# Performance work log

Measured on AMD Instinct MI355X. Metric: run time of the kernel, lower is better.

Reference implementation:

```python
import jax, jax.numpy as jnp
import numpy as np
from jax import lax

B_, K_, T_, V_ = 2, 4, 1024, 1024
D_MODEL, EXPAND = 512, 2
D_INNER = EXPAND * D_MODEL          # 1024
N_STATE, D_CONV, DT_RANK, L_ = 16, 4, 32, 2


def setup_inputs() -> dict:
    key = jax.random.key(0)
    ks = jax.random.split(key, 9)
    s = 0.02
    A0 = jnp.log(jnp.arange(1, N_STATE + 1, dtype=jnp.float32))  # S4D-real init
    return {
        'codes': jax.random.randint(ks[0], (B_, K_, T_), 0, V_),
        'embed_w': jax.random.normal(ks[1], (K_, V_, D_MODEL), jnp.float32) * s,
        'norm_w': jnp.ones((L_, D_MODEL), jnp.float32),
        'in_proj_w': jax.random.normal(ks[2], (L_, 2 * D_INNER, D_MODEL), jnp.float32) * s,
        'conv_w': jax.random.normal(ks[3], (L_, D_INNER, 1, D_CONV), jnp.float32) * s,
        'conv_b': jnp.zeros((L_, D_INNER), jnp.float32),
        'x_proj_w': jax.random.normal(ks[4], (L_, DT_RANK + 2 * N_STATE, D_INNER), jnp.float32) * s,
        'dt_proj_w': jax.random.normal(ks[5], (L_, D_INNER, DT_RANK), jnp.float32) * s,
        'dt_proj_b': jnp.zeros((L_, D_INNER), jnp.float32),
        'A_log': jnp.broadcast_to(A0, (L_, D_INNER, N_STATE)) + 0.0,
        'D_skip': jnp.ones((L_, D_INNER), jnp.float32),
        'out_proj_w': jax.random.normal(ks[6], (L_, D_MODEL, D_INNER), jnp.float32) * s,
        'head_w': jax.random.normal(ks[7], (K_, D_MODEL, V_), jnp.float32) * s,
    }


def rmsnorm(x, w, eps=1e-6):
    return x * w * lax.rsqrt(jnp.mean(x * x, axis=-1, keepdims=True) + eps)


def causal_dwconv(x, w, b):
    # x: (B,T,D); w: (D,1,d_conv) depthwise; torch pads d_conv-1 both sides then slices [:T]
    # == left-pad-only causal conv.
    xt = x.transpose(0, 2, 1)  # (B,D,T)
    y = lax.conv_general_dilated(xt, w, (1,), [(D_CONV - 1, 0)],
                                 feature_group_count=D_INNER,
                                 dimension_numbers=('NCH', 'OIH', 'NCH'))
    return (y + b[None, :, None]).transpose(0, 2, 1)


def mamba_block(x, norm_w, in_w, cw, cb, xp_w, dtp_w, dtp_b, A_log, D_skip, out_w):
    res = x
    x = rmsnorm(x, norm_w)
    xz = x @ in_w.T                                   # (B,T,2*d_inner)
    x_ssm, z = jnp.split(xz, 2, axis=-1)
    x_ssm = jax.nn.silu(causal_dwconv(x_ssm, cw, cb))  # (B,T,D)
    x_dbl = x_ssm @ xp_w.T                            # (B,T,dt_rank+2N)
    dt_lr, Bm, Cm = jnp.split(x_dbl, [DT_RANK, DT_RANK + N_STATE], axis=-1)
    dt = jax.nn.softplus(dt_lr @ dtp_w.T + dtp_b)     # (B,T,D)
    A = -jnp.exp(A_log)                               # (D,N)
    dA = jnp.exp(dt[..., None] * A)                   # (B,T,D,N)
    dBx = dt[..., None] * Bm[:, :, None, :] * x_ssm[..., None]  # (B,T,D,N)

    def step(h, inp):
        dA_t, dBx_t, C_t = inp
        h = dA_t * h + dBx_t                          # (B,D,N)
        return h, jnp.einsum('bdn,bn->bd', h, C_t)

    h0 = jnp.zeros((x.shape[0], D_INNER, N_STATE), x.dtype)
    _, ys = lax.scan(step, h0, (dA.transpose(1, 0, 2, 3),
                                dBx.transpose(1, 0, 2, 3),
                                Cm.transpose(1, 0, 2)))
    y = ys.transpose(1, 0, 2) + x_ssm * D_skip        # (B,T,D)
    y = y * jax.nn.silu(z)
    return res + y @ out_w.T


def reference(codes, embed_w, norm_w, in_proj_w, conv_w, conv_b, x_proj_w,
              dt_proj_w, dt_proj_b, A_log, D_skip, out_proj_w, head_w):
    k_idx = jnp.arange(K_)[None, :, None]
    x = embed_w[k_idx, codes].sum(axis=1)             # (B,T,d_model): RVQ sum-embedding
    for l in range(L_):
        x = mamba_block(x, norm_w[l], in_proj_w[l], conv_w[l], conv_b[l],
                        x_proj_w[l], dt_proj_w[l], dt_proj_b[l],
                        A_log[l], D_skip[l], out_proj_w[l])
    return jnp.einsum('btd,kdv->bktv', x, head_w)     # (B,K,T,V)
```

## Files before the change

### kernel.cpp

```cpp
#include <hip/hip_runtime.h>
#include <hip/hip_bf16.h>


#define B_SZ 2
#define K_CB 4
#define T_SZ 1024
#define V_SZ 1024
#define DM 512
#define DI 1024
#define NS 16
#define DTR 32
#define NCHUNK 64
#define TCHUNK 16

typedef unsigned short u16;
typedef long long ll;
using short8 = __attribute__((ext_vector_type(8))) short;
using f32x4  = __attribute__((ext_vector_type(4))) float;

__device__ __forceinline__ float bf2f(u16 u) {
    union { unsigned int i; float f; } v; v.i = ((unsigned int)u) << 16; return v.f;
}
__device__ __forceinline__ u16 f2bf(float f) {
    union { float f; unsigned int i; } v; v.f = f;
    unsigned int x = v.i;
    return (u16)((x + 0x7fffu + ((x >> 16) & 1u)) >> 16);
}
__device__ __forceinline__ float siluf(float x) { return x / (1.f + __expf(-x)); }
__device__ __forceinline__ float softplusf(float x) { return (x > 20.f) ? x : log1pf(__expf(x)); }

__global__ __launch_bounds__(256) void mega0_k(const float* __restrict__ in_w,
                                               const float* __restrict__ xp_w,
                                               const float* __restrict__ dtp_w,
                                               const float* __restrict__ out_w,
                                               u16* __restrict__ w_in, u16* __restrict__ w_xp,
                                               u16* __restrict__ w_dt, u16* __restrict__ w_out,
                                               const float* __restrict__ head_w,
                                               u16* __restrict__ w_hd,
                                               const int* __restrict__ codes,
                                               const float* __restrict__ ew,
                                               const float* __restrict__ nw,
                                               float* __restrict__ x,
                                               u16* __restrict__ xn) {
    __shared__ float tile[64][65];
    int bid = blockIdx.x;
    int tid = threadIdx.x;
    if (bid < 3264) {
        int i = (bid * 256 + tid) << 2;
        const float* s; u16* d;
        if (i < 2097152) { s = in_w + i; d = w_in + i; }
        else {
            i -= 2097152;
            if (i < 131072) { s = xp_w + i; d = w_xp + i; }
            else {
                i -= 131072;
                if (i < 65536) { s = dtp_w + i; d = w_dt + i; }
                else { i -= 65536; s = out_w + i; d = w_out + i; }
            }
        }
        float4 v = *(const float4*)s;
        ushort4 o; o.x = f2bf(v.x); o.y = f2bf(v.y); o.z = f2bf(v.z); o.w = f2bf(v.w);
        *(ushort4*)d = o;
    } else if (bid < 3776) {
        int idx = bid - 3264;
        int z = idx >> 7, rest = idx & 127;
        int d0 = (rest >> 4) << 6, v0 = (rest & 15) << 6;
        int col = tid & 63, rbase = tid >> 6;
#pragma unroll
        for (int i = 0; i < 16; i++) {
            int row = (i << 2) + rbase;
            tile[row][col] = head_w[(ll)z * (DM * V_SZ) + (ll)(d0 + row) * V_SZ + v0 + col];
        }
        __syncthreads();
#pragma unroll
        for (int i = 0; i < 16; i++) {
            int vrow = (i << 2) + rbase;
            w_hd[(ll)z * (V_SZ * DM) + (ll)(v0 + vrow) * DM + d0 + col] = f2bf(tile[col][vrow]);
        }
    } else {
        int row = bid - 3776;
        int b = row >> 10, t = row & 1023;
        float a0 = 0.f, a1 = 0.f;
#pragma unroll
        for (int k = 0; k < K_CB; k++) {
            int c = codes[b * (K_CB * T_SZ) + k * T_SZ + t];
            a0 += ew[((ll)k * V_SZ + c) * DM + tid];
            a1 += ew[((ll)k * V_SZ + c) * DM + tid + 256];
        }
        x[(ll)row * DM + tid]       = a0;
        x[(ll)row * DM + tid + 256] = a1;
        float ss = a0 * a0 + a1 * a1;
#pragma unroll
        for (int off = 32; off > 0; off >>= 1) ss += __shfl_down(ss, off, 64);
        float* red = &tile[0][0];
        if ((tid & 63) == 0) red[tid >> 6] = ss;
        __syncthreads();
        float tot = red[0] + red[1] + red[2] + red[3];
        float scale = rsqrtf(tot * (1.0f / DM) + 1e-6f);
        xn[(ll)row * DM + tid]       = f2bf(a0 * scale * nw[tid]);
        xn[(ll)row * DM + tid + 256] = f2bf(a1 * scale * nw[tid + 256]);
    }
}

__global__ __launch_bounds__(256) void rmsnorm_k(const float* __restrict__ x,
                                                 const float* __restrict__ w,
                                                 u16* __restrict__ xn) {
    ll row = blockIdx.x;
    const float* xr = x + row * DM;
    int tid = threadIdx.x;
    float v0 = xr[tid], v1 = xr[tid + 256];
    float ss = v0 * v0 + v1 * v1;
#pragma unroll
    for (int off = 32; off > 0; off >>= 1) ss += __shfl_down(ss, off, 64);
    __shared__ float red[4];
    if ((tid & 63) == 0) red[tid >> 6] = ss;
    __syncthreads();
    float tot = red[0] + red[1] + red[2] + red[3];
    float scale = rsqrtf(tot * (1.0f / DM) + 1e-6f);
    xn[row * DM + tid]       = f2bf(v0 * scale * w[tid]);
    xn[row * DM + tid + 256] = f2bf(v1 * scale * w[tid + 256]);
}

template <int EP>
__global__ __launch_bounds__(256) void mgemm2_k(const u16* __restrict__ A, int lda,
                                                const u16* __restrict__ W,
                                                float* __restrict__ C,
                                                u16* __restrict__ Cb, int ldcb, int K) {
    __shared__ u16 As[2][4096];
    __shared__ u16 Bs[2][4096];
    int tid = threadIdx.x;
    int wave = tid >> 6, lane = tid & 63;
    int q = lane >> 4, r = lane & 15;
    int m0 = blockIdx.y << 7, n0 = blockIdx.x << 7;
    int wm = (wave >> 1) << 6, wn = (wave & 1) << 6;
    int srow = tid >> 1, soff = (tid & 1) << 4;
    const u16* Ap = A + (ll)(m0 + srow) * lda + soff;
    const u16* Wp = W + (ll)(n0 + srow) * K + soff;
    int sidx = (srow << 5) + soff;
    f32x4 acc[4][4];
#pragma unroll
    for (int i = 0; i < 4; i++)
#pragma unroll
        for (int j = 0; j < 4; j++) acc[i][j] = (f32x4){0.f, 0.f, 0.f, 0.f};

    uint4 ra0 = *(const uint4*)Ap,       ra1 = *(const uint4*)(Ap + 8);
    uint4 rb0 = *(const uint4*)Wp,       rb1 = *(const uint4*)(Wp + 8);
    *(uint4*)&As[0][sidx] = ra0; *(uint4*)&As[0][sidx + 8] = ra1;
    *(uint4*)&Bs[0][sidx] = rb0; *(uint4*)&Bs[0][sidx + 8] = rb1;
    __syncthreads();

    int p = 0;
    for (int k0 = 0; k0 < K; k0 += 32) {
        bool pf = (k0 + 32) < K;
        if (pf) {
            ra0 = *(const uint4*)(Ap + k0 + 32); ra1 = *(const uint4*)(Ap + k0 + 40);
            rb0 = *(const uint4*)(Wp + k0 + 32); rb1 = *(const uint4*)(Wp + k0 + 40);
        }
        short8 af[4], bfr[4];
#pragma unroll
        for (int i = 0; i < 4; i++) af[i]  = *(const short8*)&As[p][((wm + (i << 4) + r) << 5) + (q << 3)];
#pragma unroll
        for (int j = 0; j < 4; j++) bfr[j] = *(const short8*)&Bs[p][((wn + (j << 4) + r) << 5) + (q << 3)];
#pragma unroll
        for (int i = 0; i < 4; i++)
#pragma unroll
            for (int j = 0; j < 4; j++)
                acc[i][j] = __builtin_amdgcn_mfma_f32_16x16x32_bf16(af[i], bfr[j], acc[i][j], 0, 0, 0);
        if (pf) {
            *(uint4*)&As[p ^ 1][sidx] = ra0; *(uint4*)&As[p ^ 1][sidx + 8] = ra1;
            *(uint4*)&Bs[p ^ 1][sidx] = rb0; *(uint4*)&Bs[p ^ 1][sidx + 8] = rb1;
        }
        __syncthreads();
        p ^= 1;
    }

#pragma unroll
    for (int i = 0; i < 4; i++)
#pragma unroll
        for (int j = 0; j < 4; j++)
#pragma unroll
            for (int g = 0; g < 4; g++) {
                int m = m0 + wm + (i << 4) + (q << 2) + g;
                int n = n0 + wn + (j << 4) + r;
                float v = acc[i][j][g];
                if (EP == 0) {
                    Cb[(ll)m * ldcb + n] = f2bf(v);
                } else {
                    int z = n >> 10, vv = n & 1023;
                    int b = m >> 10, t = m & 1023;
                    C[((ll)(b * K_CB + z) * T_SZ + t) * V_SZ + vv] = v;
                }
            }
}

template <int EP>
__global__ __launch_bounds__(256) void mgemm_k(const u16* __restrict__ A, int lda,
                                               const u16* __restrict__ W,
                                               float* __restrict__ C, int ldc, int K,
                                               const float* __restrict__ bias,
                                               u16* __restrict__ Cb, int ldcb) {
    __shared__ u16 As[2][2048];
    __shared__ u16 Bs[2][2048];
    int tid = threadIdx.x;
    int m0 = blockIdx.y << 6, n0 = blockIdx.x << 6;
    int lane = tid & 63, wave = tid >> 6;
    int q = lane >> 4, r = lane & 15;
    int wm = (wave >> 1) << 5, wn = (wave & 1) << 5;
    int srow = tid >> 2, soff = (tid & 3) << 3;
    const u16* Ap = A + (ll)(m0 + srow) * lda + soff;
    const u16* Wp = W + (ll)(n0 + srow) * K + soff;
    int sidx = (srow << 5) + soff;
    f32x4 acc[2][2];
#pragma unroll
    for (int i = 0; i < 2; i++)
#pragma unroll
        for (int j = 0; j < 2; j++) acc[i][j] = (f32x4){0.f, 0.f, 0.f, 0.f};

    uint4 ra = *(const uint4*)Ap;
    uint4 rb = *(const uint4*)Wp;
    *(uint4*)&As[0][sidx] = ra;
    *(uint4*)&Bs[0][sidx] = rb;
    __syncthreads();

    int p = 0;
    for (int k0 = 0; k0 < K; k0 += 32) {
        bool pf = (k0 + 32) < K;
        if (pf) {
            ra = *(const uint4*)(Ap + k0 + 32);
            rb = *(const uint4*)(Wp + k0 + 32);
        }
        short8 af[2], bfr[2];
#pragma unroll
        for (int i = 0; i < 2; i++) af[i]  = *(const short8*)&As[p][((wm + (i << 4) + r) << 5) + (q << 3)];
#pragma unroll
        for (int j = 0; j < 2; j++) bfr[j] = *(const short8*)&Bs[p][((wn + (j << 4) + r) << 5) + (q << 3)];
#pragma unroll
        for (int i = 0; i < 2; i++)
#pragma unroll
            for (int j = 0; j < 2; j++)
                acc[i][j] = __builtin_amdgcn_mfma_f32_16x16x32_bf16(af[i], bfr[j], acc[i][j], 0, 0, 0);
        if (pf) {
            *(uint4*)&As[p ^ 1][sidx] = ra;
            *(uint4*)&Bs[p ^ 1][sidx] = rb;
        }
        __syncthreads();
        p ^= 1;
    }

#pragma unroll
    for (int i = 0; i < 2; i++)
#pragma unroll
        for (int j = 0; j < 2; j++)
#pragma unroll
            for (int g = 0; g < 4; g++) {
                int m = m0 + wm + (i << 4) + (q << 2) + g;
                int n = n0 + wn + (j << 4) + r;
                float v = acc[i][j][g];
                float nv = C[(ll)m * ldc + n] + v;
                C[(ll)m * ldc + n] = nv;
                Cb[(ll)m * ldcb + n] = f2bf(nv);
            }
}

__global__ __launch_bounds__(256) void convxp_k(const u16* __restrict__ xzb,
                                                const float* __restrict__ cw,
                                                const float* __restrict__ cb,
                                                const u16* __restrict__ W,
                                                float* __restrict__ xc,
                                                float* __restrict__ xdbl,
                                                u16* __restrict__ xdbl_bf) {
    __shared__ u16 xcs[16][1032];
    __shared__ u16 Bs[2][2048];
    int blk = blockIdx.x, tid = threadIdx.x;
    int b = blk >> 6, tg = blk & 63;
    int t0 = tg << 4;
    ll ro0 = (ll)b * T_SZ + t0;
    int c0 = tid << 2;
    float4 a = *(const float4*)&cb[c0];
    float4 cwv[4];
#pragma unroll
    for (int e = 0; e < 4; e++) cwv[e] = *(const float4*)&cw[(c0 + e) << 2];
    ushort4 v[19];
#pragma unroll
    for (int i = 0; i < 19; i++) {
        int t = t0 - 3 + i;
        if (t >= 0) v[i] = *(const ushort4*)&xzb[((ll)(b * T_SZ + t)) * (2 * DI) + c0];
        else        v[i] = (ushort4){0, 0, 0, 0};
    }
#pragma unroll
    for (int tr = 0; tr < 16; tr++) {
        float acc0 = a.x, acc1 = a.y, acc2 = a.z, acc3 = a.w;
#pragma unroll
        for (int j = 0; j < 4; j++) {
            ushort4 vv = v[tr + j];
            acc0 = fmaf(bf2f(vv.x), ((const float*)&cwv[0])[j], acc0);
            acc1 = fmaf(bf2f(vv.y), ((const float*)&cwv[1])[j], acc1);
            acc2 = fmaf(bf2f(vv.z), ((const float*)&cwv[2])[j], acc2);
            acc3 = fmaf(bf2f(vv.w), ((const float*)&cwv[3])[j], acc3);
        }
        float4 s; ushort4 sb;
        s.x = siluf(acc0); s.y = siluf(acc1); s.z = siluf(acc2); s.w = siluf(acc3);
        sb.x = f2bf(s.x); sb.y = f2bf(s.y); sb.z = f2bf(s.z); sb.w = f2bf(s.w);
        *(float4*)&xc[(ro0 + tr) * DI + c0] = s;
        *(ushort4*)&xcs[tr][c0] = sb;
    }
    __syncthreads();

    int lane = tid & 63, wave = tid >> 6;
    int q = lane >> 4, r = lane & 15;
    int srow = tid >> 2, soff = (tid & 3) << 3;
    f32x4 acc = (f32x4){0.f, 0.f, 0.f, 0.f};
    uint4 rb = *(const uint4*)(W + (ll)srow * DI + soff);
    *(uint4*)&Bs[0][(srow << 5) + soff] = rb;
    __syncthreads();
    int p = 0;
    for (int k0 = 0; k0 < DI; k0 += 32) {
        bool pf = (k0 + 32) < DI;
        if (pf) rb = *(const uint4*)(W + (ll)srow * DI + k0 + 32 + soff);
        short8 af  = *(const short8*)&xcs[r][k0 + (q << 3)];
        short8 bfr = *(const short8*)&Bs[p][(((wave << 4) + r) << 5) + (q << 3)];
        acc = __builtin_amdgcn_mfma_f32_16x16x32_bf16(af, bfr, acc, 0, 0, 0);
        if (pf) *(uint4*)&Bs[p ^ 1][(srow << 5) + soff] = rb;
        __syncthreads();
        p ^= 1;
    }
#pragma unroll
    for (int g = 0; g < 4; g++) {
        int tr = (q << 2) + g;
        int n = (wave << 4) + r;
        float vv = acc[g];
        xdbl[(ro0 + tr) * 64 + n]    = vv;
        xdbl_bf[(ro0 + tr) * 64 + n] = f2bf(vv);
    }
}

__global__ __launch_bounds__(256) void dtscan1_k(const u16* __restrict__ A,
                                                 const u16* __restrict__ W,
                                                 const float* __restrict__ bias,
                                                 const float* __restrict__ xc,
                                                 const float* __restrict__ xdbl,
                                                 const float* __restrict__ A_log,
                                                 float* __restrict__ dtb,
                                                 float* __restrict__ pA,
                                                 float* __restrict__ U) {
    __shared__ u16 As[2048];
    __shared__ u16 Bs[2048];
    __shared__ float dts[64][65];
    __shared__ float BCs[64][16];
    int tid = threadIdx.x;
    int m0 = blockIdx.y << 6, n0 = blockIdx.x << 6;
    int lane = tid & 63, wave = tid >> 6;
    int q = lane >> 4, r = lane & 15;
    int wm = (wave >> 1) << 5, wn = (wave & 1) << 5;
    {
        int srow = tid >> 2, soff = (tid & 3) << 3;
        *(uint4*)&As[(srow << 5) + soff] = *(const uint4*)(A + (ll)(m0 + srow) * 64 + soff);
        *(uint4*)&Bs[(srow << 5) + soff] = *(const uint4*)(W + (ll)(n0 + srow) * DTR + soff);
        int rr = tid >> 2, cc = (tid & 3) << 2;
        *(float4*)&BCs[rr][cc] = *(const float4*)&xdbl[(ll)(m0 + rr) * 64 + DTR + cc];
    }
    int sd = lane;
    int sc = wave;
    int dg = n0 + sd;
    float Av[NS];
#pragma unroll
    for (int n4 = 0; n4 < 4; n4++) {
        float4 alv = *(const float4*)&A_log[dg * NS + (n4 << 2)];
        Av[(n4 << 2) + 0] = -__expf(alv.x); Av[(n4 << 2) + 1] = -__expf(alv.y);
        Av[(n4 << 2) + 2] = -__expf(alv.z); Av[(n4 << 2) + 3] = -__expf(alv.w);
    }
    __syncthreads();

    f32x4 acc[2][2];
#pragma unroll
    for (int i = 0; i < 2; i++)
#pragma unroll
        for (int j = 0; j < 2; j++) acc[i][j] = (f32x4){0.f, 0.f, 0.f, 0.f};
    short8 af[2], bfr[2];
#pragma unroll
    for (int i = 0; i < 2; i++) af[i]  = *(const short8*)&As[((wm + (i << 4) + r) << 5) + (q << 3)];
#pragma unroll
    for (int j = 0; j < 2; j++) bfr[j] = *(const short8*)&Bs[((wn + (j << 4) + r) << 5) + (q << 3)];
#pragma unroll
    for (int i = 0; i < 2; i++)
#pragma unroll
        for (int j = 0; j < 2; j++)
            acc[i][j] = __builtin_amdgcn_mfma_f32_16x16x32_bf16(af[i], bfr[j], acc[i][j], 0, 0, 0);

#pragma unroll
    for (int i = 0; i < 2; i++)
#pragma unroll
        for (int j = 0; j < 2; j++)
#pragma unroll
            for (int g = 0; g < 4; g++) {
                int mm = wm + (i << 4) + (q << 2) + g;
                int nn = wn + (j << 4) + r;
                float dtl = softplusf(acc[i][j][g] + bias[n0 + nn]);
                dtb[(ll)(m0 + mm) * DI + (n0 + nn)] = dtl;
                dts[mm][nn] = dtl;
            }
    __syncthreads();

    int b = m0 >> 10;
    int c = ((m0 & 1023) >> 4) + sc;
    int tl0 = sc << 4;
    float p[NS], u[NS];
#pragma unroll
    for (int n = 0; n < NS; n++) { p[n] = 1.f; u[n] = 0.f; }
#pragma unroll
    for (int s = 0; s < TCHUNK; s++) {
        int tl = tl0 + s;
        float dtv = dts[tl][sd];
        float xv = xc[(ll)(m0 + tl) * DI + dg];
        float dx = dtv * xv;
#pragma unroll
        for (int n = 0; n < NS; n++) {
            float aa = __expf(dtv * Av[n]);
            p[n] *= aa;
            u[n] = fmaf(aa, u[n], dx * BCs[tl][n]);
        }
    }
    ll o = ((ll)b * NCHUNK + c) * (NS * DI) + dg;
#pragma unroll
    for (int n = 0; n < NS; n++) { pA[o + n * DI] = p[n]; U[o + n * DI] = u[n]; }
}

__global__ __launch_bounds__(256) void scan2_k(const float* __restrict__ pA,
                                               const float* __restrict__ U,
                                               float* __restrict__ hst) {
    int i = blockIdx.x * 256 + threadIdx.x;
    int b = i >> 14;
    int rest = i & 16383;
    float h = 0.f;
#pragma unroll
    for (int c = 0; c < NCHUNK; c++) {
        ll o = ((ll)b * NCHUNK + c) * (DI * NS) + rest;
        float pa = pA[o], u = U[o];
        hst[o] = h;
        h = fmaf(pa, h, u);
    }
}

__global__ __launch_bounds__(256) void scan3_k(const float* __restrict__ dt,
                                               const float* __restrict__ xc,
                                               const float* __restrict__ xdbl,
                                               const u16* __restrict__ xzb,
                                               const float* __restrict__ A_log,
                                               const float* __restrict__ Dk,
                                               const float* __restrict__ hst,
                                               u16* __restrict__ y) {
    int blk = blockIdx.x;
    int dblk = blk & 3;
    int c = (blk >> 2) & (NCHUNK - 1);
    int b = blk >> 8;
    int d = dblk * 256 + threadIdx.x;
    int t0 = c * TCHUNK;
    __shared__ float BC[TCHUNK][32];
    if (threadIdx.x < TCHUNK * 8) {
        int rr = threadIdx.x >> 3, cc = (threadIdx.x & 7) << 2;
        *(float4*)&BC[rr][cc] = *(const float4*)&xdbl[((ll)(b * T_SZ + t0 + rr)) * 64 + DTR + cc];
    }
    float Av[NS];
#pragma unroll
    for (int n4 = 0; n4 < 4; n4++) {
        float4 alv = *(const float4*)&A_log[d * NS + (n4 << 2)];
        Av[(n4 << 2) + 0] = -__expf(alv.x); Av[(n4 << 2) + 1] = -__expf(alv.y);
        Av[(n4 << 2) + 2] = -__expf(alv.z); Av[(n4 << 2) + 3] = -__expf(alv.w);
    }
    float h[NS];
    ll ho = (((ll)b * NCHUNK + c) * (NS * DI)) + d;
#pragma unroll
    for (int n = 0; n < NS; n++) h[n] = hst[ho + n * DI];
    float Dv = Dk[d];
    __syncthreads();
#pragma unroll
    for (int s = 0; s < TCHUNK; s++) {
        ll ro = (ll)(b * T_SZ + t0 + s);
        float dtv = dt[ro * DI + d];
        float xv = xc[ro * DI + d];
        float dx = dtv * xv;
        float acc = 0.f;
#pragma unroll
        for (int n = 0; n < NS; n++) {
            float aa = __expf(dtv * Av[n]);
            h[n] = fmaf(aa, h[n], dx * BC[s][n]);
            acc = fmaf(h[n], BC[s][16 + n], acc);
        }
        float zv = bf2f(xzb[ro * (2 * DI) + DI + d]);
        y[ro * DI + d] = f2bf((acc + xv * Dv) * siluf(zv));
    }
}

extern "C" void kernel_launch(void* const* d_in, const int* in_sizes, int n_in,
                              void* d_out, int out_size, void* d_ws, size_t ws_size,
                              hipStream_t stream) {
    const int*   codes   = (const int*)d_in[0];
    const float* embed_w = (const float*)d_in[1];
    const float* norm_w  = (const float*)d_in[2];
    const float* in_w    = (const float*)d_in[3];
    const float* conv_w  = (const float*)d_in[4];
    const float* conv_b  = (const float*)d_in[5];
    const float* xp_w    = (const float*)d_in[6];
    const float* dtp_w   = (const float*)d_in[7];
    const float* dtp_b   = (const float*)d_in[8];
    const float* A_log   = (const float*)d_in[9];
    const float* D_skip  = (const float*)d_in[10];
    const float* out_w   = (const float*)d_in[11];
    const float* head_w  = (const float*)d_in[12];
    float* out = (float*)d_out;

    float* ws = (float*)d_ws;
    float* x    = ws;
    float* xc   = x + 1048576;
    float* dtb  = xc + 2097152;
    float* xdbl = dtb + 2097152;
    float* pA   = xdbl + 131072;
    float* Uh   = pA + 2097152;

    u16* us       = (u16*)(Uh + 2097152);
    u16* xz_bf    = us;
    u16* xbf      = xz_bf + 4194304;
    u16* ybxn_bf  = xbf + 2097152;
    u16* xdbl_bf  = ybxn_bf + 2097152;
    u16* w_in_bf  = xdbl_bf + 131072;
    u16* w_xp_bf  = w_in_bf + 2097152;
    u16* w_dt_bf  = w_xp_bf + 131072;
    u16* w_out_bf = w_dt_bf + 65536;
    u16* w_hd_bf  = w_out_bf + 1048576;

    u16* xn_bf = ybxn_bf;
    u16* y_bf  = ybxn_bf;
    u16* x_bf  = xbf;

    mega0_k<<<5824, 256, 0, stream>>>(in_w, xp_w, dtp_w, out_w,
                                      w_in_bf, w_xp_bf, w_dt_bf, w_out_bf,
                                      head_w, w_hd_bf, codes, embed_w, norm_w, x, xn_bf);

    for (int l = 0; l < 2; l++) {
        const float* al = A_log + l * DI * NS;
        if (l == 1)
            rmsnorm_k<<<2048, 256, 0, stream>>>(x, norm_w + DM, xn_bf);
        mgemm2_k<0><<<dim3(16, 16), 256, 0, stream>>>(xn_bf, DM, w_in_bf + l * 1048576,
                                                      nullptr, xz_bf, 2 * DI, DM);
        convxp_k<<<128, 256, 0, stream>>>(xz_bf, conv_w + l * DI * 4, conv_b + l * DI,
                                          w_xp_bf + l * 65536, xc, xdbl, xdbl_bf);
        dtscan1_k<<<dim3(16, 32), 256, 0, stream>>>(xdbl_bf, w_dt_bf + l * 32768,
                                                    dtp_b + l * DI, xc, xdbl, al,
                                                    dtb, pA, Uh);
        scan2_k<<<128, 256, 0, stream>>>(pA, Uh, Uh);
        scan3_k<<<512, 256, 0, stream>>>(dtb, xc, xdbl, xz_bf, al, D_skip + l * DI, Uh, y_bf);
        mgemm_k<3><<<dim3(8, 32), 256, 0, stream>>>(y_bf, DI, w_out_bf + l * 524288,
                                                    x, DM, DI, nullptr, x_bf, DM);
    }

    mgemm2_k<4><<<dim3(32, 16), 256, 0, stream>>>(x_bf, DM, w_hd_bf, out, nullptr, 0, DM);
}
```

Before: 282.2 us.

## Fuse layer-1 RMSNorm into out_proj epilogue and in_proj GEMM scaling

Removes the standalone rmsnorm kernel before layer 1. The norm weight is folded into the layer-1 in_proj weights during conversion. The layer-0 out_proj epilogue accumulates per-row sums of squares via shuffles and atomics into a buffer zeroed by the setup kernel. The layer-1 in_proj GEMM then takes the un-normalized bf16 residual and applies the rsqrt scale per row in its epilogue. This saves one launch and a pass over x, but adds atomics, and normalizing after the bf16 GEMM changes rounding slightly.

```diff
diff --git a/kernel.cpp b/kernel.cpp
--- a/kernel.cpp
+++ b/kernel.cpp
@@ -41,15 +41,20 @@
                                                const float* __restrict__ ew,
                                                const float* __restrict__ nw,
                                                float* __restrict__ x,
-                                               u16* __restrict__ xn) {
+                                               u16* __restrict__ xn,
+                                               float* __restrict__ rs_sum) {
     __shared__ float tile[64][65];
     int bid = blockIdx.x;
     int tid = threadIdx.x;
     if (bid < 3264) {
-        int i = (bid * 256 + tid) << 2;
+        int i0 = (bid * 256 + tid) << 2;
+        int i = i0;
         const float* s; u16* d;
-        if (i < 2097152) { s = in_w + i; d = w_in + i; }
-        else {
+        bool in_w_l1 = false;
+        if (i < 2097152) {
+            s = in_w + i; d = w_in + i;
+            in_w_l1 = (i >= 1048576);
+        } else {
             i -= 2097152;
             if (i < 131072) { s = xp_w + i; d = w_xp + i; }
             else {
@@ -59,6 +64,11 @@
             }
         }
         float4 v = *(const float4*)s;
+        if (in_w_l1) {
+            int k = i0 & 511;
+            const float* nr = nw + DM;
+            v.x *= nr[k]; v.y *= nr[k + 1]; v.z *= nr[k + 2]; v.w *= nr[k + 3];
+        }
         ushort4 o; o.x = f2bf(v.x); o.y = f2bf(v.y); o.z = f2bf(v.z); o.w = f2bf(v.w);
         *(ushort4*)d = o;
     } else if (bid < 3776) {
@@ -77,7 +87,7 @@
             int vrow = (i << 2) + rbase;
             w_hd[(ll)z * (V_SZ * DM) + (ll)(v0 + vrow) * DM + d0 + col] = f2bf(tile[col][vrow]);
         }
-    } else {
+    } else if (bid < 5824) {
         int row = bid - 3776;
         int b = row >> 10, t = row & 1023;
         float a0 = 0.f, a1 = 0.f;
@@ -99,33 +109,18 @@
         float scale = rsqrtf(tot * (1.0f / DM) + 1e-6f);
         xn[(ll)row * DM + tid]       = f2bf(a0 * scale * nw[tid]);
         xn[(ll)row * DM + tid + 256] = f2bf(a1 * scale * nw[tid + 256]);
-    }
-}
-
-__global__ __launch_bounds__(256) void rmsnorm_k(const float* __restrict__ x,
-                                                 const float* __restrict__ w,
-                                                 u16* __restrict__ xn) {
-    ll row = blockIdx.x;
-    const float* xr = x + row * DM;
-    int tid = threadIdx.x;
-    float v0 = xr[tid], v1 = xr[tid + 256];
-    float ss = v0 * v0 + v1 * v1;
-#pragma unroll
-    for (int off = 32; off > 0; off >>= 1) ss += __shfl_down(ss, off, 64);
-    __shared__ float red[4];
-    if ((tid & 63) == 0) red[tid >> 6] = ss;
-    __syncthreads();
-    float tot = red[0] + red[1] + red[2] + red[3];
-    float scale = rsqrtf(tot * (1.0f / DM) + 1e-6f);
-    xn[row * DM + tid]       = f2bf(v0 * scale * w[tid]);
-    xn[row * DM + tid + 256] = f2bf(v1 * scale * w[tid + 256]);
+    } else {
+        int i = (bid - 5824) * 1024 + tid * 4;
+        *(float4*)&rs_sum[i] = (float4){0.f, 0.f, 0.f, 0.f};
+    }
 }
 
 template <int EP>
 __global__ __launch_bounds__(256) void mgemm2_k(const u16* __restrict__ A, int lda,
                                                 const u16* __restrict__ W,
                                                 float* __restrict__ C,
-                                                u16* __restrict__ Cb, int ldcb, int K) {
+                                                u16* __restrict__ Cb, int ldcb, int K,
+                                                const float* __restrict__ rs) {
     __shared__ u16 As[2][4096];
     __shared__ u16 Bs[2][4096];
     int tid = threadIdx.x;
@@ -185,6 +180,9 @@
                 float v = acc[i][j][g];
                 if (EP == 0) {
                     Cb[(ll)m * ldcb + n] = f2bf(v);
+                } else if (EP == 5) {
+                    float sc = rsqrtf(rs[m] * (1.0f / DM) + 1e-6f);
+                    Cb[(ll)m * ldcb + n] = f2bf(v * sc);
                 } else {
                     int z = n >> 10, vv = n & 1023;
                     int b = m >> 10, t = m & 1023;
@@ -198,7 +196,8 @@
                                                const u16* __restrict__ W,
                                                float* __restrict__ C, int ldc, int K,
                                                const float* __restrict__ bias,
-                                               u16* __restrict__ Cb, int ldcb) {
+                                               u16* __restrict__ Cb, int ldcb,
+                                               float* __restrict__ rs) {
     __shared__ u16 As[2][2048];
     __shared__ u16 Bs[2][2048];
     int tid = threadIdx.x;
@@ -250,16 +249,24 @@
 #pragma unroll
     for (int i = 0; i < 2; i++)
 #pragma unroll
-        for (int j = 0; j < 2; j++)
-#pragma unroll
-            for (int g = 0; g < 4; g++) {
+        for (int g = 0; g < 4; g++) {
+            float s = 0.f;
+#pragma unroll
+            for (int j = 0; j < 2; j++) {
                 int m = m0 + wm + (i << 4) + (q << 2) + g;
                 int n = n0 + wn + (j << 4) + r;
                 float v = acc[i][j][g];
                 float nv = C[(ll)m * ldc + n] + v;
                 C[(ll)m * ldc + n] = nv;
                 Cb[(ll)m * ldcb + n] = f2bf(nv);
+                if (EP == 6) s += nv * nv;
             }
+            if (EP == 6) {
+#pragma unroll
+                for (int off = 8; off > 0; off >>= 1) s += __shfl_xor(s, off, 64);
+                if (r == 0) atomicAdd(&rs[m0 + wm + (i << 4) + (q << 2) + g], s);
+            }
+        }
 }
 
 __global__ __launch_bounds__(256) void convxp_k(const u16* __restrict__ xzb,
@@ -516,8 +523,9 @@
     float* xdbl = dtb + 2097152;
     float* pA   = xdbl + 131072;
     float* Uh   = pA + 2097152;
-
-    u16* us       = (u16*)(Uh + 2097152);
+    float* rs_sum = Uh + 2097152;
+
+    u16* us       = (u16*)(rs_sum + 2048);
     u16* xz_bf    = us;
     u16* xbf      = xz_bf + 4194304;
     u16* ybxn_bf  = xbf + 2097152;
@@ -532,16 +540,19 @@
     u16* y_bf  = ybxn_bf;
     u16* x_bf  = xbf;
 
-    mega0_k<<<5824, 256, 0, stream>>>(in_w, xp_w, dtp_w, out_w,
+    mega0_k<<<5826, 256, 0, stream>>>(in_w, xp_w, dtp_w, out_w,
                                       w_in_bf, w_xp_bf, w_dt_bf, w_out_bf,
-                                      head_w, w_hd_bf, codes, embed_w, norm_w, x, xn_bf);
+                                      head_w, w_hd_bf, codes, embed_w, norm_w, x, xn_bf,
+                                      rs_sum);
 
     for (int l = 0; l < 2; l++) {
         const float* al = A_log + l * DI * NS;
-        if (l == 1)
-            rmsnorm_k<<<2048, 256, 0, stream>>>(x, norm_w + DM, xn_bf);
-        mgemm2_k<0><<<dim3(16, 16), 256, 0, stream>>>(xn_bf, DM, w_in_bf + l * 1048576,
-                                                      nullptr, xz_bf, 2 * DI, DM);
+        if (l == 0)
+            mgemm2_k<0><<<dim3(16, 16), 256, 0, stream>>>(xn_bf, DM, w_in_bf,
+                                                          nullptr, xz_bf, 2 * DI, DM, nullptr);
+        else
+            mgemm2_k<5><<<dim3(16, 16), 256, 0, stream>>>(x_bf, DM, w_in_bf + 1048576,
+                                                          nullptr, xz_bf, 2 * DI, DM, rs_sum);
         convxp_k<<<128, 256, 0, stream>>>(xz_bf, conv_w + l * DI * 4, conv_b + l * DI,
                                           w_xp_bf + l * 65536, xc, xdbl, xdbl_bf);
         dtscan1_k<<<dim3(16, 32), 256, 0, stream>>>(xdbl_bf, w_dt_bf + l * 32768,
@@ -549,9 +560,13 @@
                                                     dtb, pA, Uh);
         scan2_k<<<128, 256, 0, stream>>>(pA, Uh, Uh);
         scan3_k<<<512, 256, 0, stream>>>(dtb, xc, xdbl, xz_bf, al, D_skip + l * DI, Uh, y_bf);
-        mgemm_k<3><<<dim3(8, 32), 256, 0, stream>>>(y_bf, DI, w_out_bf + l * 524288,
-                                                    x, DM, DI, nullptr, x_bf, DM);
-    }
-
-    mgemm2_k<4><<<dim3(32, 16), 256, 0, stream>>>(x_bf, DM, w_hd_bf, out, nullptr, 0, DM);
-}
+        if (l == 0)
+            mgemm_k<6><<<dim3(8, 32), 256, 0, stream>>>(y_bf, DI, w_out_bf,
+                                                        x, DM, DI, nullptr, x_bf, DM, rs_sum);
+        else
+            mgemm_k<3><<<dim3(8, 32), 256, 0, stream>>>(y_bf, DI, w_out_bf + 524288,
+                                                        x, DM, DI, nullptr, x_bf, DM, nullptr);
+    }
+
+    mgemm2_k<4><<<dim3(32, 16), 256, 0, stream>>>(x_bf, DM, w_hd_bf, out, nullptr, 0, DM, nullptr);
+}
```

Result: slower. 322.4 us (+14.2%).
